# Performance work log

Hardware: AMD Instinct MI355X
Metric: run time of the kernel (lower is better)

The kernel has to match this reference:

```python
import jax, jax.numpy as jnp
import numpy as np

IN, HID, BATCH = 1024, 1024, 4096


def _linear_params(key, out_dim, in_dim):
    # torch.nn.Linear default init: U(-1/sqrt(in), 1/sqrt(in))
    k1, k2 = jax.random.split(key)
    bound = 1.0 / np.sqrt(in_dim)
    w = jax.random.uniform(k1, (out_dim, in_dim), jnp.float32, -bound, bound)
    b = jax.random.uniform(k2, (out_dim,), jnp.float32, -bound, bound)
    return w, b


def setup_inputs() -> dict:
    key = jax.random.key(0)
    keys = jax.random.split(key, 11)
    inp = {
        'input': jax.random.normal(keys[0], (BATCH, IN), jnp.float32),
        'h': jax.random.normal(keys[1], (BATCH, HID), jnp.float32),
        'c': jax.random.normal(keys[2], (BATCH, HID), jnp.float32),
    }
    names = ['i_i', 'i_h', 'f_i', 'f_h', 'g_i', 'g_h', 'o_i', 'o_h']
    for n, k in zip(names, keys[3:]):
        in_dim = IN if n.endswith('_i') else HID
        w, b = _linear_params(k, HID, in_dim)
        inp['w_' + n] = w
        inp['b_' + n] = b
    return inp


def reference(input, h, c,
              w_i_i, b_i_i, w_i_h, b_i_h,
              w_f_i, b_f_i, w_f_h, b_f_h,
              w_g_i, b_g_i, w_g_h, b_g_h,
              w_o_i, b_o_i, w_o_h, b_o_h):
    def lin(x, w, b):
        return x @ w.T + b

    i = jax.nn.sigmoid(lin(input, w_i_i, b_i_i) + lin(h, w_i_h, b_i_h))
    f = jax.nn.sigmoid(lin(input, w_f_i, b_f_i) + lin(h, w_f_h, b_f_h))
    g = jnp.tanh(lin(input, w_g_i, b_g_i) + lin(h, w_g_h, b_g_h))
    o = jax.nn.sigmoid(lin(input, w_o_i, b_o_i) + lin(h, w_o_h, b_o_h))
    c_prime = f * c + i * g
    h_prime = o * jnp.tanh(c_prime)
    return (h_prime, c_prime)
```

## Files before the change

kernel.cpp:

```cpp
#include <hip/hip_runtime.h>
#include <stdint.h>

#define BATCH 4096
#define IN_DIM 1024
#define HID 1024
#define KDIM 2048
#define NGATE 4096
#define BK 64
#define BM 256
#define BN 256
#define NT (KDIM / BK)
#define EPITCH2 264

typedef __attribute__((ext_vector_type(4))) float floatx4;
typedef __attribute__((ext_vector_type(8))) __bf16 bf16x8;
typedef __attribute__((ext_vector_type(8))) unsigned short ushort8;

__device__ __forceinline__ unsigned short f2bf(float f) {
    union { float f; unsigned int u; } v; v.f = f;
    unsigned int u = v.u;
    u += 0x7fffu + ((u >> 16) & 1u);
    return (unsigned short)(u >> 16);
}
__device__ __forceinline__ float bf2f(unsigned short s) {
    union { unsigned int u; float f; } v; v.u = ((unsigned int)s) << 16;
    return v.f;
}
__device__ __forceinline__ ushort8 cvt8(const float* __restrict__ src) {
    float4 v0 = ((const float4*)src)[0];
    float4 v1 = ((const float4*)src)[1];
    ushort8 o = { f2bf(v0.x), f2bf(v0.y), f2bf(v0.z), f2bf(v0.w),
                  f2bf(v1.x), f2bf(v1.y), f2bf(v1.z), f2bf(v1.w) };
    return o;
}

__global__ __launch_bounds__(256) void prep_kernel(
    const float* __restrict__ x,  const float* __restrict__ h,
    const float* __restrict__ wii, const float* __restrict__ wih,
    const float* __restrict__ wfi, const float* __restrict__ wfh,
    const float* __restrict__ wgi, const float* __restrict__ wgh,
    const float* __restrict__ woi, const float* __restrict__ woh,
    const float* __restrict__ bii, const float* __restrict__ bih,
    const float* __restrict__ bfi, const float* __restrict__ bfh,
    const float* __restrict__ bgi, const float* __restrict__ bgh,
    const float* __restrict__ boi, const float* __restrict__ boh,
    unsigned short* __restrict__ Xb,
    unsigned short* __restrict__ Wb,
    float* __restrict__ bias)
{
    const int bid = blockIdx.x;
    const int tid = threadIdx.x;

    if (bid < 2048) {
        const int e = (bid * 256 + tid) * 8;
        const int b = e >> 10, k = e & 1023;
        *(ushort8*)(Xb + (size_t)b * KDIM + k) = cvt8(x + e);
    } else if (bid < 4096) {
        const int e = ((bid - 2048) * 256 + tid) * 8;
        const int b = e >> 10, k = e & 1023;
        *(ushort8*)(Xb + (size_t)b * KDIM + 1024 + k) = cvt8(h + e);
    } else if (bid < 8192) {
        const int m   = (bid - 4096) >> 9;
        const int off = (bid - 4096) & 511;
        const int e = (off * 256 + tid) * 8;
        const int n = e >> 10, k = e & 1023;
        const float* src;
        switch (m) {
            case 0: src = wii; break; case 1: src = wih; break;
            case 2: src = wfi; break; case 3: src = wfh; break;
            case 4: src = wgi; break; case 5: src = wgh; break;
            case 6: src = woi; break; default: src = woh; break;
        }
        const int gate = m >> 1, part = m & 1;
        *(ushort8*)(Wb + (size_t)(n * 4 + gate) * KDIM + part * 1024 + k)
            = cvt8(src + e);
    } else {
        const int t = (bid - 8192) * 256 + tid;
        const int gate = (bid - 8192) >> 2;
        const int n = t & 1023;
        const float *bi, *bh_;
        switch (gate) {
            case 0: bi = bii; bh_ = bih; break;
            case 1: bi = bfi; bh_ = bfh; break;
            case 2: bi = bgi; bh_ = bgh; break;
            default: bi = boi; bh_ = boh; break;
        }
        bias[n * 4 + gate] = bi[n] + bh_[n];
    }
}

#define GLD16(g, l)                                                          \
    __builtin_amdgcn_global_load_lds(                                        \
        (__attribute__((address_space(1))) void*)(g),                        \
        (__attribute__((address_space(3))) void*)(l), 16, 0, 0)
#define BAR()     asm volatile("s_barrier" ::: "memory")
#define VMCNT(n)  asm volatile("s_waitcnt vmcnt(" #n ")" ::: "memory")

__global__ __launch_bounds__(512, 2) void gemm_lstm(
    const unsigned short* __restrict__ X,
    const unsigned short* __restrict__ W,
    const float* __restrict__ bias,
    const float* __restrict__ c_in,
    float* __restrict__ out)
{
    __shared__ __align__(16) unsigned char smem[131072];
    unsigned short* sA[2][2];
    unsigned short* sB[2][2];
#pragma unroll
    for (int b_ = 0; b_ < 2; ++b_)
#pragma unroll
        for (int h_ = 0; h_ < 2; ++h_) {
            sA[b_][h_] = (unsigned short*)(smem + ((b_ * 2 + h_) << 14));
            sB[b_][h_] = (unsigned short*)(smem + 65536 + ((b_ * 2 + h_) << 14));
        }

    const int tid  = threadIdx.x;
    const int wave = tid >> 6;
    const int lane = tid & 63;
    const int idx  = lane & 15;
    const int quad = lane >> 4;
    const int wrow = wave >> 2;
    const int wcol = wave & 3;

    const int l   = blockIdx.x;
    const int xcd = l & 7;
    const int s   = l >> 3;
    const int bx  = xcd * 2 + (s >> 4);
    const int by  = s & 15;
    const int rowA0 = bx * BM;
    const int rowB0 = by * BN;

    const int srow = tid >> 3;
    const int skk  = ((tid & 7) ^ (srow & 7)) * 8;
    const unsigned short* gA = X + (size_t)(rowA0 + srow) * KDIM + skk;
    const unsigned short* gB = W + (size_t)(rowB0 + srow) * KDIM + skk;

#define STAGE_A(buf, ht, kt) do {                                             \
    GLD16(gA + ((size_t)((ht) * 128)) * KDIM + (size_t)(kt) * 64,             \
          sA[buf][ht] + tid * 8);                                             \
    GLD16(gA + ((size_t)((ht) * 128 + 64)) * KDIM + (size_t)(kt) * 64,        \
          sA[buf][ht] + 4096 + tid * 8);                                      \
  } while (0)
#define STAGE_B(buf, ht, kt) do {                                             \
    GLD16(gB + ((size_t)((ht) * 128)) * KDIM + (size_t)(kt) * 64,             \
          sB[buf][ht] + tid * 8);                                             \
    GLD16(gB + ((size_t)((ht) * 128 + 64)) * KDIM + (size_t)(kt) * 64,        \
          sB[buf][ht] + 4096 + tid * 8);                                      \
  } while (0)

    const int aoff = (wrow * 64 + idx) * 64;
    const int boff = (wcol * 32 + idx) * 64;
    const int co0  = (quad ^ (idx & 7)) * 8;
    const int co1  = ((4 + quad) ^ (idx & 7)) * 8;

    bf16x8 af[4][2], bfr[2][2];
    floatx4 acc[2][2][4][2] = {};

#define RD_A(buf, MH) do {                                                    \
    const unsigned short* pA_ = sA[buf][MH] + aoff;                           \
    _Pragma("unroll") for (int i_ = 0; i_ < 4; ++i_) {                        \
        af[i_][0] = *(const bf16x8*)(pA_ + i_ * 1024 + co0);                  \
        af[i_][1] = *(const bf16x8*)(pA_ + i_ * 1024 + co1); }                \
  } while (0)
#define RD_B(buf, NH) do {                                                    \
    const unsigned short* pB_ = sB[buf][NH] + boff;                           \
    _Pragma("unroll") for (int j_ = 0; j_ < 2; ++j_) {                        \
        bfr[j_][0] = *(const bf16x8*)(pB_ + j_ * 1024 + co0);                 \
        bfr[j_][1] = *(const bf16x8*)(pB_ + j_ * 1024 + co1); }               \
  } while (0)
#define MM(MH, NH) do {                                                       \
    __builtin_amdgcn_s_setprio(1);                                            \
    _Pragma("unroll") for (int i_ = 0; i_ < 4; ++i_)                          \
    _Pragma("unroll") for (int j_ = 0; j_ < 2; ++j_) {                        \
        acc[MH][NH][i_][j_] = __builtin_amdgcn_mfma_f32_16x16x32_bf16(        \
            af[i_][0], bfr[j_][0], acc[MH][NH][i_][j_], 0, 0, 0);             \
        acc[MH][NH][i_][j_] = __builtin_amdgcn_mfma_f32_16x16x32_bf16(        \
            af[i_][1], bfr[j_][1], acc[MH][NH][i_][j_], 0, 0, 0); }           \
    __builtin_amdgcn_s_setprio(0);                                            \
  } while (0)

    STAGE_A(0, 0, 0); STAGE_B(0, 0, 0); STAGE_B(0, 1, 0); STAGE_A(0, 1, 0);
    STAGE_A(1, 0, 1); STAGE_B(1, 1, 1); STAGE_A(1, 1, 1);
    VMCNT(6);
    BAR();

    for (int t0 = 0; t0 < NT - 2; t0 += 2) {
        const int t1 = t0 + 1;
        RD_A(0, 0); RD_B(0, 0); STAGE_B(1, 0, t1);     BAR(); MM(0, 0); BAR();
        RD_B(0, 1);             STAGE_A(0, 0, t0 + 2); BAR(); MM(0, 1); BAR();
        RD_A(0, 1);             STAGE_B(0, 1, t0 + 2); BAR(); MM(1, 1); BAR();
        RD_B(0, 0);             STAGE_A(0, 1, t0 + 2); VMCNT(6);
                                                       BAR(); MM(1, 0); BAR();
        RD_A(1, 0); RD_B(1, 0); STAGE_B(0, 0, t0 + 2); BAR(); MM(0, 0); BAR();
        RD_B(1, 1);             STAGE_A(1, 0, t1 + 2); BAR(); MM(0, 1); BAR();
        RD_A(1, 1);             STAGE_B(1, 1, t1 + 2); BAR(); MM(1, 1); BAR();
        RD_B(1, 0);             STAGE_A(1, 1, t1 + 2); VMCNT(6);
                                                       BAR(); MM(1, 0); BAR();
    }
    {
        RD_A(0, 0); RD_B(0, 0); STAGE_B(1, 0, NT - 1); BAR(); MM(0, 0); BAR();
        RD_B(0, 1);                                    BAR(); MM(0, 1); BAR();
        RD_A(0, 1);                                    BAR(); MM(1, 1); BAR();
        RD_B(0, 0);             VMCNT(0);              BAR(); MM(1, 0); BAR();
        RD_A(1, 0); RD_B(1, 0);                        BAR(); MM(0, 0); BAR();
        RD_B(1, 1);                                    BAR(); MM(0, 1); BAR();
        RD_A(1, 1);                                    BAR(); MM(1, 1); BAR();
        RD_B(1, 0);                                    BAR(); MM(1, 0); BAR();
    }

    unsigned short* E = (unsigned short*)smem;
    const int gate   = idx & 3;
    const int rowo16 = tid >> 4;
    const int t16    = tid & 15;
    float* __restrict__ out_h = out;
    float* __restrict__ out_c = out + (size_t)BATCH * HID;

#pragma unroll
    for (int half = 0; half < 2; ++half) {
#pragma unroll
        for (int nh = 0; nh < 2; ++nh) {
#pragma unroll
            for (int j = 0; j < 2; ++j) {
                const int col = nh * 128 + wcol * 32 + j * 16 + idx;
                const float bv = bias[rowB0 + col];
#pragma unroll
                for (int i = 0; i < 4; ++i) {
#pragma unroll
                    for (int r = 0; r < 4; ++r) {
                        const int row = wrow * 64 + i * 16 + quad * 4 + r;
                        const float v = ((half == 0) ? acc[0][nh][i][j][r]
                                                     : acc[1][nh][i][j][r]) + bv;
                        const float vv = (gate == 2) ? 2.f * v : v;
                        const float s2 = 1.f / (1.f + __expf(-vv));
                        const float a  = (gate == 2) ? 2.f * s2 - 1.f : s2;
                        E[row * EPITCH2 + col] = f2bf(a);
                    }
                }
            }
        }
        __syncthreads();

#pragma unroll
        for (int p = 0; p < 4; ++p) {
            const int row_l = p * 32 + rowo16;
            const int row_g = rowA0 + half * 128 + row_l;
            const int colc  = t16 * 16;
            ushort8 e0 = *(const ushort8*)(E + row_l * EPITCH2 + colc);
            ushort8 e1 = *(const ushort8*)(E + row_l * EPITCH2 + colc + 8);
            const int u0 = (rowB0 >> 2) + t16 * 4;
            const float4 cv = *(const float4*)(c_in + (size_t)row_g * HID + u0);

            float cvv[4] = { cv.x, cv.y, cv.z, cv.w };
            float hp[4], cp[4];
#pragma unroll
            for (int d = 0; d < 4; ++d) {
                const ushort8& e = (d < 2) ? e0 : e1;
                const int b = (d & 1) * 4;
                const float iv = bf2f(e[b + 0]);
                const float fv = bf2f(e[b + 1]);
                const float gv = bf2f(e[b + 2]);
                const float ov = bf2f(e[b + 3]);
                const float c2 = fv * cvv[d] + iv * gv;
                const float e2 = __expf(2.f * c2);
                cp[d] = c2;
                hp[d] = ov * ((e2 - 1.f) / (e2 + 1.f));
            }
            float4 hv  = { hp[0], hp[1], hp[2], hp[3] };
            float4 cpv = { cp[0], cp[1], cp[2], cp[3] };
            *(float4*)(out_h + (size_t)row_g * HID + u0) = hv;
            *(float4*)(out_c + (size_t)row_g * HID + u0) = cpv;
        }
        __syncthreads();
    }
}

extern "C" void kernel_launch(void* const* d_in, const int* in_sizes, int n_in,
                              void* d_out, int out_size, void* d_ws, size_t ws_size,
                              hipStream_t stream) {
    const float* x   = (const float*)d_in[0];
    const float* h   = (const float*)d_in[1];
    const float* c   = (const float*)d_in[2];
    const float* wii = (const float*)d_in[3];
    const float* bii = (const float*)d_in[4];
    const float* wih = (const float*)d_in[5];
    const float* bih = (const float*)d_in[6];
    const float* wfi = (const float*)d_in[7];
    const float* bfi = (const float*)d_in[8];
    const float* wfh = (const float*)d_in[9];
    const float* bfh = (const float*)d_in[10];
    const float* wgi = (const float*)d_in[11];
    const float* bgi = (const float*)d_in[12];
    const float* wgh = (const float*)d_in[13];
    const float* bgh = (const float*)d_in[14];
    const float* woi = (const float*)d_in[15];
    const float* boi = (const float*)d_in[16];
    const float* woh = (const float*)d_in[17];
    const float* boh = (const float*)d_in[18];

    char* ws = (char*)d_ws;
    unsigned short* Xb  = (unsigned short*)ws;
    unsigned short* Wb  = (unsigned short*)(ws + ((size_t)16 << 20));
    float*          bsv = (float*)(ws + ((size_t)32 << 20));

    prep_kernel<<<8208, 256, 0, stream>>>(
        x, h, wii, wih, wfi, wfh, wgi, wgh, woi, woh,
        bii, bih, bfi, bfh, bgi, bgh, boi, boh, Xb, Wb, bsv);

    gemm_lstm<<<(BATCH / BM) * (NGATE / BN), 512, 0, stream>>>(
        Xb, Wb, bsv, c, (float*)d_out);
}
```

Before: 215.1 us.

## Double-buffer B fragments and halve barriers in GEMM main loop

Adds a second B-fragment register set so each A read feeds two MFMA blocks back to back. The staging order changes so each phase issues two global-to-LDS loads and then a single wait plus barrier, replacing the two barriers around every MM step. The goal is less barrier and LDS-read stall time between MFMA bursts. It raises register pressure under 512-thread, 2-block launch bounds, and the reworked LDS buffer reuse ordering could introduce races if the waits are wrong.

```diff
diff --git a/kernel.cpp b/kernel.cpp
--- a/kernel.cpp
+++ b/kernel.cpp
@@ -95,6 +95,7 @@
         (__attribute__((address_space(3))) void*)(l), 16, 0, 0)
 #define BAR()     asm volatile("s_barrier" ::: "memory")
 #define VMCNT(n)  asm volatile("s_waitcnt vmcnt(" #n ")" ::: "memory")
+#define WAITL0()  asm volatile("s_waitcnt lgkmcnt(0)" ::: "memory")
 
 __global__ __launch_bounds__(512, 2) void gemm_lstm(
     const unsigned short* __restrict__ X,
@@ -153,7 +154,7 @@
     const int co0  = (quad ^ (idx & 7)) * 8;
     const int co1  = ((4 + quad) ^ (idx & 7)) * 8;
 
-    bf16x8 af[4][2], bfr[2][2];
+    bf16x8 af[4][2], bfr0[2][2], bfr1[2][2];
     floatx4 acc[2][2][4][2] = {};
 
 #define RD_A(buf, MH) do {                                                    \
@@ -162,50 +163,62 @@
         af[i_][0] = *(const bf16x8*)(pA_ + i_ * 1024 + co0);                  \
         af[i_][1] = *(const bf16x8*)(pA_ + i_ * 1024 + co1); }                \
   } while (0)
-#define RD_B(buf, NH) do {                                                    \
+#define RD_B(dst, buf, NH) do {                                               \
     const unsigned short* pB_ = sB[buf][NH] + boff;                           \
     _Pragma("unroll") for (int j_ = 0; j_ < 2; ++j_) {                        \
-        bfr[j_][0] = *(const bf16x8*)(pB_ + j_ * 1024 + co0);                 \
-        bfr[j_][1] = *(const bf16x8*)(pB_ + j_ * 1024 + co1); }               \
-  } while (0)
-#define MM(MH, NH) do {                                                       \
+        dst[j_][0] = *(const bf16x8*)(pB_ + j_ * 1024 + co0);                 \
+        dst[j_][1] = *(const bf16x8*)(pB_ + j_ * 1024 + co1); }               \
+  } while (0)
+#define MM(MH, NH, BFR) do {                                                  \
     __builtin_amdgcn_s_setprio(1);                                            \
     _Pragma("unroll") for (int i_ = 0; i_ < 4; ++i_)                          \
     _Pragma("unroll") for (int j_ = 0; j_ < 2; ++j_) {                        \
         acc[MH][NH][i_][j_] = __builtin_amdgcn_mfma_f32_16x16x32_bf16(        \
-            af[i_][0], bfr[j_][0], acc[MH][NH][i_][j_], 0, 0, 0);             \
+            af[i_][0], BFR[j_][0], acc[MH][NH][i_][j_], 0, 0, 0);             \
         acc[MH][NH][i_][j_] = __builtin_amdgcn_mfma_f32_16x16x32_bf16(        \
-            af[i_][1], bfr[j_][1], acc[MH][NH][i_][j_], 0, 0, 0); }           \
+            af[i_][1], BFR[j_][1], acc[MH][NH][i_][j_], 0, 0, 0); }           \
     __builtin_amdgcn_s_setprio(0);                                            \
   } while (0)
 
     STAGE_A(0, 0, 0); STAGE_B(0, 0, 0); STAGE_B(0, 1, 0); STAGE_A(0, 1, 0);
-    STAGE_A(1, 0, 1); STAGE_B(1, 1, 1); STAGE_A(1, 1, 1);
-    VMCNT(6);
+    STAGE_A(1, 0, 1); STAGE_B(1, 1, 1);
+    VMCNT(4);
     BAR();
 
-    for (int t0 = 0; t0 < NT - 2; t0 += 2) {
+    for (int t0 = 0; t0 <= NT - 4; t0 += 2) {
         const int t1 = t0 + 1;
-        RD_A(0, 0); RD_B(0, 0); STAGE_B(1, 0, t1);     BAR(); MM(0, 0); BAR();
-        RD_B(0, 1);             STAGE_A(0, 0, t0 + 2); BAR(); MM(0, 1); BAR();
-        RD_A(0, 1);             STAGE_B(0, 1, t0 + 2); BAR(); MM(1, 1); BAR();
-        RD_B(0, 0);             STAGE_A(0, 1, t0 + 2); VMCNT(6);
-                                                       BAR(); MM(1, 0); BAR();
-        RD_A(1, 0); RD_B(1, 0); STAGE_B(0, 0, t0 + 2); BAR(); MM(0, 0); BAR();
-        RD_B(1, 1);             STAGE_A(1, 0, t1 + 2); BAR(); MM(0, 1); BAR();
-        RD_A(1, 1);             STAGE_B(1, 1, t1 + 2); BAR(); MM(1, 1); BAR();
-        RD_B(1, 0);             STAGE_A(1, 1, t1 + 2); VMCNT(6);
-                                                       BAR(); MM(1, 0); BAR();
+        RD_A(0, 0); RD_B(bfr0, 0, 0); RD_B(bfr1, 0, 1);
+        STAGE_B(1, 0, t1); STAGE_A(1, 1, t1);
+        MM(0, 0, bfr0); MM(0, 1, bfr1);
+        VMCNT(4); BAR();
+        RD_A(0, 1); RD_B(bfr0, 0, 0);
+        STAGE_A(0, 0, t0 + 2); STAGE_B(0, 1, t0 + 2);
+        MM(1, 1, bfr1); MM(1, 0, bfr0);
+        VMCNT(4); BAR();
+        RD_A(1, 0); RD_B(bfr0, 1, 0); RD_B(bfr1, 1, 1);
+        STAGE_B(0, 0, t0 + 2); STAGE_A(0, 1, t0 + 2);
+        MM(0, 0, bfr0); MM(0, 1, bfr1);
+        VMCNT(4); BAR();
+        RD_A(1, 1); RD_B(bfr0, 1, 0);
+        STAGE_A(1, 0, t1 + 2); STAGE_B(1, 1, t1 + 2);
+        MM(1, 1, bfr1); MM(1, 0, bfr0);
+        VMCNT(4); BAR();
     }
     {
-        RD_A(0, 0); RD_B(0, 0); STAGE_B(1, 0, NT - 1); BAR(); MM(0, 0); BAR();
-        RD_B(0, 1);                                    BAR(); MM(0, 1); BAR();
-        RD_A(0, 1);                                    BAR(); MM(1, 1); BAR();
-        RD_B(0, 0);             VMCNT(0);              BAR(); MM(1, 0); BAR();
-        RD_A(1, 0); RD_B(1, 0);                        BAR(); MM(0, 0); BAR();
-        RD_B(1, 1);                                    BAR(); MM(0, 1); BAR();
-        RD_A(1, 1);                                    BAR(); MM(1, 1); BAR();
-        RD_B(1, 0);                                    BAR(); MM(1, 0); BAR();
+        RD_A(0, 0); RD_B(bfr0, 0, 0); RD_B(bfr1, 0, 1);
+        STAGE_B(1, 0, NT - 1); STAGE_A(1, 1, NT - 1);
+        MM(0, 0, bfr0); MM(0, 1, bfr1);
+        VMCNT(4); BAR();
+        RD_A(0, 1); RD_B(bfr0, 0, 0);
+        MM(1, 1, bfr1); MM(1, 0, bfr0);
+        VMCNT(0); BAR();
+        RD_A(1, 0); RD_B(bfr0, 1, 0); RD_B(bfr1, 1, 1);
+        MM(0, 0, bfr0); MM(0, 1, bfr1);
+        BAR();
+        RD_A(1, 1); RD_B(bfr0, 1, 0);
+        MM(1, 1, bfr1); MM(1, 0, bfr0);
+        WAITL0();
+        BAR();
     }
 
     unsigned short* E = (unsigned short*)smem;
```

Result: no change. 216.1 us (+0.5%).
